# Optimization experiments

Measured on AMD Instinct MI355X. Metric: run time of the kernel, lower is better.

## Reference

```python
import jax, jax.numpy as jnp
import numpy as np

N = 50000      # nodes
E = 600000     # edges
G = 256        # graphs in batch
HID = 128      # gcn hidden = gcn in = gcn out
EDIM = 16      # edge feature dim
EH = 64        # edge mlp hidden
NL = 4         # gcn layers
MIN_ = 200     # mol feature dim
MH = 256       # mlp hidden
MOUT = 128     # mlp out
PH = 512       # predictor hidden
PIN = HID + MOUT


def setup_inputs() -> dict:
    key = jax.random.key(0)
    ks = jax.random.split(key, 32)
    f = lambda k, s: jax.random.normal(k, s, dtype=jnp.float32)
    p = lambda k, s: 0.05 * jax.random.normal(k, s, dtype=jnp.float32)
    return {
        "x": f(ks[0], (N, HID)),
        "edge_index": jax.random.randint(ks[1], (2, E), 0, N),
        "edge_attr": f(ks[2], (E, EDIM)),
        "batch_index": jnp.sort(jax.random.randint(ks[3], (N,), 0, G)),
        "mol_features": f(ks[4], (G, MIN_)),
        # PDNConv params (stacked over NL layers)
        "conv_lin_W": p(ks[5], (NL, HID, HID)),
        "conv_mW1": p(ks[6], (NL, EDIM, EH)),
        "conv_mb1": p(ks[7], (NL, EH)),
        "conv_mW2": p(ks[8], (NL, EH)),
        "conv_mb2": p(ks[9], (NL,)),
        "conv_bias": p(ks[10], (NL, HID)),
        # dense Linear after each conv
        "gcn_W": p(ks[11], (NL, HID, HID)),
        "gcn_b": p(ks[12], (NL, HID)),
        # mol-feature MLP (n_mlp_layers=3 -> 4 linears)
        "mlp_W0": p(ks[13], (MIN_, MH)), "mlp_b0": p(ks[14], (MH,)),
        "mlp_W1": p(ks[15], (MH, MH)),   "mlp_b1": p(ks[16], (MH,)),
        "mlp_W2": p(ks[17], (MH, MH)),   "mlp_b2": p(ks[18], (MH,)),
        "mlp_W3": p(ks[19], (MH, MOUT)), "mlp_b3": p(ks[20], (MOUT,)),
        # predictor
        "pred_W0": p(ks[21], (PIN, PH)), "pred_b0": p(ks[22], (PH,)),
        "pred_W1": p(ks[23], (PH, PH)),  "pred_b1": p(ks[24], (PH,)),
        "out_W": p(ks[25], (PH, 1)),     "out_b": p(ks[26], (1,)),
    }


def _pdn_conv(h, row, col, edge_attr, lin_W, mW1, mb1, mW2, mb2, bias):
    # edge MLP -> sigmoid gate (PyG PDNConv)
    w = jax.nn.sigmoid(jnp.maximum(edge_attr @ mW1 + mb1, 0.0) @ mW2 + mb2)  # [E]
    # gcn_norm with self loops (fill weight 1.0)
    loop = jnp.arange(N)
    r = jnp.concatenate([row, loop])
    c = jnp.concatenate([col, loop])
    w_all = jnp.concatenate([w, jnp.ones((N,), h.dtype)])
    deg = jax.ops.segment_sum(w_all, c, num_segments=N)
    dinv = jnp.where(deg > 0, jax.lax.rsqrt(deg), 0.0)
    norm = dinv[r] * w_all * dinv[c]                                          # [E+N]
    hl = h @ lin_W                                                            # [N,HID]
    out = jax.ops.segment_sum(norm[:, None] * hl[r], c, num_segments=N)
    return out + bias


def reference(x, edge_index, edge_attr, batch_index, mol_features,
              conv_lin_W, conv_mW1, conv_mb1, conv_mW2, conv_mb2, conv_bias,
              gcn_W, gcn_b,
              mlp_W0, mlp_b0, mlp_W1, mlp_b1, mlp_W2, mlp_b2, mlp_W3, mlp_b3,
              pred_W0, pred_b0, pred_W1, pred_b1, out_W, out_b):
    row, col = edge_index[0], edge_index[1]
    relu = lambda v: jnp.maximum(v, 0.0)

    # GCN stack: PDNConv -> relu(Linear), x NL
    h1 = x
    for i in range(NL):
        h1 = _pdn_conv(h1, row, col, edge_attr, conv_lin_W[i], conv_mW1[i],
                       conv_mb1[i], conv_mW2[i], conv_mb2[i], conv_bias[i])
        h1 = relu(h1 @ gcn_W[i] + gcn_b[i])
    # global mean pool over graphs
    sums = jax.ops.segment_sum(h1, batch_index, num_segments=G)
    cnts = jax.ops.segment_sum(jnp.ones((N,), h1.dtype), batch_index, num_segments=G)
    h1 = sums / jnp.maximum(cnts, 1.0)[:, None]                               # [G,HID]

    # molecular-feature MLP
    h2 = relu(mol_features @ mlp_W0 + mlp_b0)
    h2 = relu(h2 @ mlp_W1 + mlp_b1)
    h2 = relu(h2 @ mlp_W2 + mlp_b2)
    h2 = relu(h2 @ mlp_W3 + mlp_b3)                                           # [G,MOUT]

    h = jnp.concatenate([h1, h2], axis=1)                                     # [G,PIN]
    h = relu(h @ pred_W0 + pred_b0)
    h = relu(h @ pred_W1 + pred_b1)
    return h @ out_W + out_b                                                  # [G,1]
```

## Files before the change

### kernel.cpp

```cpp
#include <hip/hip_runtime.h>
#include <hip/hip_bf16.h>


#define NN 50000
#define EE 600000
#define GG 256
#define HID 128
#define EDIM 16
#define EHID 64
#define NL 4
#define MIN_F 200
#define MH 256
#define MOUT 128
#define PH 512
#define PIN 256
#define SCAN_B 196
#define PCH 8

typedef __hip_bfloat16 bf16;
typedef __attribute__((ext_vector_type(8))) short bf16x8;
typedef __attribute__((ext_vector_type(4))) float f32x4;

__device__ __forceinline__ float bfl(unsigned u) { return __uint_as_float(u << 16); }
__device__ __forceinline__ float bfh(unsigned u) { return __uint_as_float(u & 0xffff0000u); }
__device__ __forceinline__ float b2f(bf16 x) { return __bfloat162float(x); }
__device__ __forceinline__ float ldf(const void* p, long i, bool bf) {
  return bf ? __bfloat162float(((const bf16*)p)[i]) : ((const float*)p)[i];
}
__device__ __forceinline__ unsigned short f2bf_bits(float v) {
  bf16 h = __float2bfloat16(v);
  return *reinterpret_cast<unsigned short*>(&h);
}

__global__ void probe_kernel(const unsigned short* __restrict__ xs, int* flag) {
  if (threadIdx.x == 0 && blockIdx.x == 0) {
    int sane = 0;
    for (int i = 0; i < 128; i++) {
      unsigned e = (xs[i] >> 7) & 0xFF;
      if (e >= 96 && e <= 159) sane++;
    }
    *flag = (sane >= 112) ? 1 : 0;
  }
}

__global__ __launch_bounds__(256) void cvt_to_bf16(const void* __restrict__ in,
                                                   unsigned short* __restrict__ outp,
                                                   int n8, const int* __restrict__ flag) {
  bool bf = *flag != 0;
  int i = blockIdx.x * 256 + threadIdx.x;
  if (i >= n8) return;
  if (bf) {
    reinterpret_cast<uint4*>(outp)[i] = reinterpret_cast<const uint4*>(in)[i];
  } else {
    const float4* p = reinterpret_cast<const float4*>(in) + (size_t)i * 2;
    float4 v0 = p[0], v1 = p[1];
    ushort4 a, b;
    a.x = f2bf_bits(v0.x); a.y = f2bf_bits(v0.y);
    a.z = f2bf_bits(v0.z); a.w = f2bf_bits(v0.w);
    b.x = f2bf_bits(v1.x); b.y = f2bf_bits(v1.y);
    b.z = f2bf_bits(v1.z); b.w = f2bf_bits(v1.w);
    reinterpret_cast<ushort4*>(outp)[i * 2] = a;
    reinterpret_cast<ushort4*>(outp)[i * 2 + 1] = b;
  }
}

__global__ __launch_bounds__(256) void cvt_molf(const void* __restrict__ in,
                                                float* __restrict__ outp,
                                                const int* __restrict__ flag) {
  bool bf = *flag != 0;
  int i = blockIdx.x * 256 + threadIdx.x;
  if (i >= GG * 50) return;
  int row = i / 50, c4 = (i % 50) * 4;
  float4 v;
  if (bf) {
    const unsigned short* p = (const unsigned short*)in + (size_t)row * MIN_F + c4;
    uint2 u = *reinterpret_cast<const uint2*>(p);
    v.x = bfl(u.x); v.y = bfh(u.x); v.z = bfl(u.y); v.w = bfh(u.y);
  } else {
    v = *reinterpret_cast<const float4*>((const float*)in + (size_t)row * MIN_F + c4);
  }
  *reinterpret_cast<float4*>(&outp[(size_t)row * 256 + c4]) = v;
}

__global__ __launch_bounds__(256) void prep_fused_w(const void* __restrict__ lin_W,
                                                    const void* __restrict__ gW,
                                                    unsigned short* __restrict__ Wt,
                                                    const int* __restrict__ flag) {
  bool bf = *flag != 0;
  int idx = blockIdx.x * 256 + threadIdx.x;
  if (idx >= 4 * 16384) return;
  int l = idx >> 14;
  int rem = idx & 16383;
  int n = rem >> 7, k = rem & 127;
  float s = 0.f;
  long lb = (long)l * 16384;
  for (int m = 0; m < 128; m++)
    s += ldf(lin_W, lb + (long)k * 128 + m, bf) * ldf(gW, lb + (long)m * 128 + n, bf);
  Wt[idx] = f2bf_bits(s);
}

__global__ __launch_bounds__(128) void prep_fused_b(const void* __restrict__ cbias,
                                                    const void* __restrict__ gW,
                                                    const void* __restrict__ gb,
                                                    float* __restrict__ bprime,
                                                    const int* __restrict__ flag) {
  bool bf = *flag != 0;
  int idx = blockIdx.x * 128 + threadIdx.x;
  if (idx >= NL * HID) return;
  int l = idx >> 7, n = idx & 127;
  float s = ldf(gb, idx, bf);
  long lb = (long)l * 16384;
  for (int k = 0; k < 128; k++)
    s += ldf(cbias, (long)l * 128 + k, bf) * ldf(gW, lb + (long)k * 128 + n, bf);
  bprime[idx] = s;
}

__global__ __launch_bounds__(256) void prep_edge_w(const void* __restrict__ mW1,
                                                   const void* __restrict__ mb1,
                                                   unsigned short* __restrict__ W1t,
                                                   const int* __restrict__ flag) {
  bool bf = *flag != 0;
  int idx = blockIdx.x * 256 + threadIdx.x;
  if (idx >= 256 * 32) return;
  int col = idx >> 5, k = idx & 31;
  float v = 0.f;
  if (k < EDIM) v = ldf(mW1, (long)(col >> 6) * (EDIM * EHID) + (long)k * EHID + (col & 63), bf);
  else if (k == EDIM) v = ldf(mb1, col, bf);
  W1t[idx] = f2bf_bits(v);
}

__global__ __launch_bounds__(256) void prep_tail(
    const void* __restrict__ mlpW0, const void* __restrict__ mlpW1,
    const void* __restrict__ mlpW2, const void* __restrict__ mlpW3,
    const void* __restrict__ predW0, const void* __restrict__ predW1,
    unsigned short* __restrict__ T, const int* __restrict__ flag) {
  bool bf = *flag != 0;
  int idx = blockIdx.x * 256 + threadIdx.x;
  const void* src; int N, Kp, Ksrc, off;
  if      (idx < 65536)  { src = mlpW0;  N = 256; Kp = 256; Ksrc = 200; off = 0; }
  else if (idx < 131072) { src = mlpW1;  N = 256; Kp = 256; Ksrc = 256; off = 65536; }
  else if (idx < 196608) { src = mlpW2;  N = 256; Kp = 256; Ksrc = 256; off = 131072; }
  else if (idx < 229376) { src = mlpW3;  N = 128; Kp = 256; Ksrc = 256; off = 196608; }
  else if (idx < 360448) { src = predW0; N = 512; Kp = 256; Ksrc = 256; off = 229376; }
  else if (idx < 622592) { src = predW1; N = 512; Kp = 512; Ksrc = 512; off = 360448; }
  else return;
  int rem = idx - off;
  int n = rem / Kp, k = rem % Kp;
  float v = (k < Ksrc) ? ldf(src, (long)k * N + n, bf) : 0.f;
  T[idx] = f2bf_bits(v);
}

__global__ __launch_bounds__(256) void count_kernel(const int* __restrict__ ei,
                                                    int* __restrict__ cnt) {
  int e = blockIdx.x * 256 + threadIdx.x;
  if (e >= EE) return;
  int c = ei[EE + e];
  c = min(max(c, 0), NN - 1);
  atomicAdd(&cnt[c], 1);
}

__global__ __launch_bounds__(256) void scan_phase1(const int* __restrict__ cnt,
                                                   int* __restrict__ bsum) {
  __shared__ int red[256];
  int tid = threadIdx.x;
  int i = blockIdx.x * 256 + tid;
  red[tid] = (i < NN) ? cnt[i] : 0;
  __syncthreads();
  for (int off = 128; off > 0; off >>= 1) {
    if (tid < off) red[tid] += red[tid + off];
    __syncthreads();
  }
  if (tid == 0) bsum[blockIdx.x] = red[0];
}

__global__ __launch_bounds__(256) void scan_phase2(int* __restrict__ bsum,
                                                   int* __restrict__ offs) {
  __shared__ int buf[256];
  int tid = threadIdx.x;
  int v = (tid < SCAN_B) ? bsum[tid] : 0;
  buf[tid] = v;
  __syncthreads();
  for (int off = 1; off < 256; off <<= 1) {
    int t = (tid >= off) ? buf[tid - off] : 0;
    __syncthreads();
    buf[tid] += t;
    __syncthreads();
  }
  if (tid < SCAN_B) bsum[tid] = buf[tid] - v;
  if (tid == 255) offs[NN] = buf[255];
}

__global__ __launch_bounds__(256) void scan_phase3(const int* __restrict__ cnt,
                                                   const int* __restrict__ bsum,
                                                   int* __restrict__ offs) {
  __shared__ int buf[256];
  int tid = threadIdx.x;
  int i = blockIdx.x * 256 + tid;
  int v = (i < NN) ? cnt[i] : 0;
  buf[tid] = v;
  __syncthreads();
  for (int off = 1; off < 256; off <<= 1) {
    int t = (tid >= off) ? buf[tid - off] : 0;
    __syncthreads();
    buf[tid] += t;
    __syncthreads();
  }
  if (i < NN) offs[i] = bsum[blockIdx.x] + buf[tid] - v;
}

__global__ __launch_bounds__(256) void fill_kernel(const int* __restrict__ ei,
                                                   const int* __restrict__ offs,
                                                   int* __restrict__ cursor,
                                                   int2* __restrict__ csr_se) {
  int e = blockIdx.x * 256 + threadIdx.x;
  if (e >= EE) return;
  int c = ei[EE + e];
  c = min(max(c, 0), NN - 1);
  int pos = offs[c] + atomicAdd(&cursor[c], 1);
  pos = min(max(pos, 0), EE - 1);
  csr_se[pos] = make_int2(ei[e], e);
}

__global__ __launch_bounds__(256) void edge_mlp_mfma(
    const void* __restrict__ eattr, const unsigned short* __restrict__ W1t,
    const void* __restrict__ mW2, const void* __restrict__ mb2,
    float* __restrict__ w_all4, const int* __restrict__ flag) {
  bool bf = *flag != 0;
  int tid = threadIdx.x;
  int wave = tid >> 6, lane = tid & 63;
  int l15 = lane & 15, quad = lane >> 4;

  bf16x8 bfrag[16];
#pragma unroll
  for (int t = 0; t < 16; t++)
    bfrag[t] = *reinterpret_cast<const bf16x8*>(&W1t[(t * 16 + l15) * 32 + quad * 8]);

  float w2v[16];
#pragma unroll
  for (int t = 0; t < 16; t++) w2v[t] = ldf(mW2, t * 16 + l15, bf);
  float b2v0 = ldf(mb2, 0, bf), b2v1 = ldf(mb2, 1, bf);
  float b2v2 = ldf(mb2, 2, bf), b2v3 = ldf(mb2, 3, bf);
  float b2 = b2v0;
  b2 = (l15 == 1) ? b2v1 : b2;
  b2 = (l15 == 2) ? b2v2 : b2;
  b2 = (l15 == 3) ? b2v3 : b2;
  bool o1 = (l15 & 1) != 0;
  bool o2 = (l15 & 2) != 0;

  int ebase = blockIdx.x * 512 + wave * 128;
#pragma unroll 1
  for (int f = 0; f < 8; f++) {
    int fbase = ebase + f * 16;
    if (fbase < EE) {
      long erow = fbase + l15;
      bf16x8 a = (bf16x8){0, 0, 0, 0, 0, 0, 0, 0};
      if (quad < 2) {
        if (bf) {
          uint4 v = *reinterpret_cast<const uint4*>((const bf16*)eattr + erow * EDIM + quad * 8);
          a = *reinterpret_cast<bf16x8*>(&v);
        } else {
          const float4* p =
              reinterpret_cast<const float4*>((const float*)eattr + erow * EDIM + quad * 8);
          float4 v0 = p[0], v1 = p[1];
          a[0] = (short)f2bf_bits(v0.x); a[1] = (short)f2bf_bits(v0.y);
          a[2] = (short)f2bf_bits(v0.z); a[3] = (short)f2bf_bits(v0.w);
          a[4] = (short)f2bf_bits(v1.x); a[5] = (short)f2bf_bits(v1.y);
          a[6] = (short)f2bf_bits(v1.z); a[7] = (short)f2bf_bits(v1.w);
        }
      }
      if (quad == 2) a[0] = (short)0x3F80;
      float s00 = 0.f, s01 = 0.f, s02 = 0.f, s03 = 0.f;
      float s10 = 0.f, s11 = 0.f, s12 = 0.f, s13 = 0.f;
      float s20 = 0.f, s21 = 0.f, s22 = 0.f, s23 = 0.f;
      float s30 = 0.f, s31 = 0.f, s32 = 0.f, s33 = 0.f;
#define DO_T(T, S0, S1, S2, S3)                                               \
  {                                                                           \
    f32x4 acc = __builtin_amdgcn_mfma_f32_16x16x32_bf16(                      \
        a, bfrag[T], (f32x4){0.f, 0.f, 0.f, 0.f}, 0, 0, 0);                   \
    S0 += fmaxf(acc.x, 0.f) * w2v[T];                                         \
    S1 += fmaxf(acc.y, 0.f) * w2v[T];                                         \
    S2 += fmaxf(acc.z, 0.f) * w2v[T];                                         \
    S3 += fmaxf(acc.w, 0.f) * w2v[T];                                         \
  }
      DO_T(0,  s00, s01, s02, s03) DO_T(1,  s00, s01, s02, s03)
      DO_T(2,  s00, s01, s02, s03) DO_T(3,  s00, s01, s02, s03)
      DO_T(4,  s10, s11, s12, s13) DO_T(5,  s10, s11, s12, s13)
      DO_T(6,  s10, s11, s12, s13) DO_T(7,  s10, s11, s12, s13)
      DO_T(8,  s20, s21, s22, s23) DO_T(9,  s20, s21, s22, s23)
      DO_T(10, s20, s21, s22, s23) DO_T(11, s20, s21, s22, s23)
      DO_T(12, s30, s31, s32, s33) DO_T(13, s30, s31, s32, s33)
      DO_T(14, s30, s31, s32, s33) DO_T(15, s30, s31, s32, s33)
#undef DO_T
#define RS_STEP1(AR, S0R, S1R) \
  float AR = (o1 ? S1R : S0R) + __shfl_xor(o1 ? S0R : S1R, 1);
      RS_STEP1(a0, s00, s10)
      RS_STEP1(a1, s01, s11)
      RS_STEP1(a2, s02, s12)
      RS_STEP1(a3, s03, s13)
      RS_STEP1(bb0, s20, s30)
      RS_STEP1(bb1, s21, s31)
      RS_STEP1(bb2, s22, s32)
      RS_STEP1(bb3, s23, s33)
#undef RS_STEP1
      float c0 = (o2 ? bb0 : a0) + __shfl_xor(o2 ? a0 : bb0, 2);
      float c1 = (o2 ? bb1 : a1) + __shfl_xor(o2 ? a1 : bb1, 2);
      float c2 = (o2 ? bb2 : a2) + __shfl_xor(o2 ? a2 : bb2, 2);
      float c3 = (o2 ? bb3 : a3) + __shfl_xor(o2 ? a3 : bb3, 2);
      c0 += __shfl_xor(c0, 4); c1 += __shfl_xor(c1, 4);
      c2 += __shfl_xor(c2, 4); c3 += __shfl_xor(c3, 4);
      c0 += __shfl_xor(c0, 8); c1 += __shfl_xor(c1, 8);
      c2 += __shfl_xor(c2, 8); c3 += __shfl_xor(c3, 8);
      if (l15 < NL) {
        float g0 = 1.f / (1.f + __expf(-(c0 + b2)));
        float g1 = 1.f / (1.f + __expf(-(c1 + b2)));
        float g2 = 1.f / (1.f + __expf(-(c2 + b2)));
        float g3 = 1.f / (1.f + __expf(-(c3 + b2)));
        w_all4[(size_t)(fbase + quad * 4 + 0) * 4 + l15] = g0;
        w_all4[(size_t)(fbase + quad * 4 + 1) * 4 + l15] = g1;
        w_all4[(size_t)(fbase + quad * 4 + 2) * 4 + l15] = g2;
        w_all4[(size_t)(fbase + quad * 4 + 3) * 4 + l15] = g3;
      }
    }
  }
}

__global__ __launch_bounds__(256) void csr_gather(const int2* __restrict__ csr_se,
                                                  const float* __restrict__ w_all4,
                                                  float* __restrict__ csr_val) {
  int k = blockIdx.x * 256 + threadIdx.x;
  if (k >= EE) return;
  int eid = csr_se[k].y;
  eid = min(max(eid, 0), EE - 1);
  float4 w = reinterpret_cast<const float4*>(w_all4)[eid];
  csr_val[k] = w.x;
  csr_val[(size_t)EE + k] = w.y;
  csr_val[2 * (size_t)EE + k] = w.z;
  csr_val[3 * (size_t)EE + k] = w.w;
}

__global__ __launch_bounds__(256) void deg_kernel(const int* __restrict__ offs,
                                                  const float* __restrict__ csr_val,
                                                  float* __restrict__ dinv4) {
  int n = blockIdx.x * 256 + threadIdx.x;
  if (n >= NN) return;
  int s = offs[n], e = offs[n + 1];
  float d0 = 1.f, d1 = 1.f, d2 = 1.f, d3 = 1.f;
  for (int k = s; k < e; k++) {
    d0 += csr_val[k];
    d1 += csr_val[EE + k];
    d2 += csr_val[2 * (size_t)EE + k];
    d3 += csr_val[3 * (size_t)EE + k];
  }
  float4 o;
  o.x = rsqrtf(d0); o.y = rsqrtf(d1); o.z = rsqrtf(d2); o.w = rsqrtf(d3);
  reinterpret_cast<float4*>(dinv4)[n] = o;
}

__global__ __launch_bounds__(256) void csr_scale_kernel(const int2* __restrict__ csr_se,
                                                        const float* __restrict__ dinv4,
                                                        float* __restrict__ csr_val) {
  int k = blockIdx.x * 256 + threadIdx.x;
  if (k >= EE) return;
  int s = csr_se[k].x;
  s = min(max(s, 0), NN - 1);
  float4 d = reinterpret_cast<const float4*>(dinv4)[s];
  csr_val[k] *= d.x;
  csr_val[(size_t)EE + k] *= d.y;
  csr_val[2 * (size_t)EE + k] *= d.z;
  csr_val[3 * (size_t)EE + k] *= d.w;
}

__global__ __launch_bounds__(256) void gemm_nodes_bf16(
    const unsigned short* __restrict__ A16, const unsigned short* __restrict__ Wt,
    const float* __restrict__ bias, unsigned short* __restrict__ out16,
    int relu) {
  __shared__ alignas(16) unsigned short sA[64 * 136];
  __shared__ alignas(16) unsigned short sW[128 * 136];
  int tid = threadIdx.x;
  int rbase = blockIdx.x * 64;

#pragma unroll
  for (int p = 0; p < 8; p++) {
    int idx8 = p * 256 + tid;
    int n = idx8 >> 4, kc = idx8 & 15;
    uint4 v = reinterpret_cast<const uint4*>(Wt)[idx8];
    *reinterpret_cast<uint4*>(&sW[n * 136 + kc * 8]) = v;
  }
#pragma unroll
  for (int p = 0; p < 4; p++) {
    int idx8 = p * 256 + tid;
    int m = idx8 >> 4, kc = idx8 & 15;
    int row = rbase + m;
    uint4 v = make_uint4(0u, 0u, 0u, 0u);
    if (row < NN)
      v = *reinterpret_cast<const uint4*>(&A16[(size_t)row * HID + kc * 8]);
    *reinterpret_cast<uint4*>(&sA[m * 136 + kc * 8]) = v;
  }
  __syncthreads();

  int wave = tid >> 6, lane = tid & 63;
  int l15 = lane & 15, quad = lane >> 4;
  int mstrip = wave * 16;

  f32x4 acc[8];
#pragma unroll
  for (int t = 0; t < 8; t++) acc[t] = (f32x4){0.f, 0.f, 0.f, 0.f};

#pragma unroll
  for (int ks = 0; ks < 4; ks++) {
    int k0 = ks * 32 + quad * 8;
    bf16x8 a = *reinterpret_cast<const bf16x8*>(&sA[(mstrip + l15) * 136 + k0]);
#pragma unroll
    for (int t = 0; t < 8; t++) {
      bf16x8 b = *reinterpret_cast<const bf16x8*>(&sW[(t * 16 + l15) * 136 + k0]);
      acc[t] = __builtin_amdgcn_mfma_f32_16x16x32_bf16(a, b, acc[t], 0, 0, 0);
    }
  }

#pragma unroll
  for (int t = 0; t < 8; t++) {
    int n = t * 16 + l15;
    float bv = bias ? bias[n] : 0.f;
#pragma unroll
    for (int r = 0; r < 4; r++) {
      int row = rbase + mstrip + quad * 4 + r;
      if (row < NN) {
        float o = acc[t][r] + bv;
        if (relu) o = fmaxf(o, 0.f);
        out16[(size_t)row * HID + n] = f2bf_bits(o);
      }
    }
  }
}

__global__ __launch_bounds__(256) void gemm_tail_mfma(
    const float* __restrict__ A, int lda, const unsigned short* __restrict__ Wt,
    int Kp, const void* __restrict__ bias, float* __restrict__ outp, int ldo,
    int relu, const int* __restrict__ flag) {
  __shared__ alignas(16) unsigned short sA[64 * 264];
  __shared__ alignas(16) unsigned short sW[64 * 264];
  int tid = threadIdx.x;
  int rbase = blockIdx.x * 64;
  int nbase = blockIdx.y * 64;
  int wave = tid >> 6, lane = tid & 63;
  int l15 = lane & 15, quad = lane >> 4;
  int mstrip = wave * 16;

  f32x4 acc[4];
#pragma unroll
  for (int t = 0; t < 4; t++) acc[t] = (f32x4){0.f, 0.f, 0.f, 0.f};

  for (int kc = 0; kc < Kp; kc += 256) {
#pragma unroll 4
    for (int p = 0; p < 16; p++) {
      int idx = p * 1024 + tid * 4;
      int m = idx >> 8, k = idx & 255;
      float4 v = *reinterpret_cast<const float4*>(&A[(size_t)(rbase + m) * lda + kc + k]);
      ushort4 b;
      b.x = f2bf_bits(v.x); b.y = f2bf_bits(v.y);
      b.z = f2bf_bits(v.z); b.w = f2bf_bits(v.w);
      *reinterpret_cast<ushort4*>(&sA[m * 264 + k]) = b;
    }
#pragma unroll 4
    for (int p = 0; p < 8; p++) {
      int idx8 = p * 256 + tid;
      int n = idx8 >> 5, kk = (idx8 & 31) * 8;
      uint4 v = *reinterpret_cast<const uint4*>(&Wt[(size_t)(nbase + n) * Kp + kc + kk]);
      *reinterpret_cast<uint4*>(&sW[n * 264 + kk]) = v;
    }
    __syncthreads();
#pragma unroll
    for (int ks = 0; ks < 8; ks++) {
      int k0 = ks * 32 + quad * 8;
      bf16x8 a = *reinterpret_cast<const bf16x8*>(&sA[(mstrip + l15) * 264 + k0]);
#pragma unroll
      for (int nt = 0; nt < 4; nt++) {
        bf16x8 b = *reinterpret_cast<const bf16x8*>(&sW[(nt * 16 + l15) * 264 + k0]);
        acc[nt] = __builtin_amdgcn_mfma_f32_16x16x32_bf16(a, b, acc[nt], 0, 0, 0);
      }
    }
    __syncthreads();
  }

  bool bf = *flag != 0;
#pragma unroll
  for (int nt = 0; nt < 4; nt++) {
    int col = nbase + nt * 16 + l15;
    float bv = ldf(bias, col, bf);
#pragma unroll
    for (int r = 0; r < 4; r++) {
      int row = rbase + mstrip + quad * 4 + r;
      float o = acc[nt][r] + bv;
      if (relu) o = fmaxf(o, 0.f);
      outp[(size_t)row * ldo + col] = o;
    }
  }
}

__global__ __launch_bounds__(64) void aggregate_kernel(
    const unsigned short* __restrict__ h16, const int* __restrict__ offs,
    const int2* __restrict__ csr_se, const float* __restrict__ csr_val,
    const float* __restrict__ dinv4, int layer,
    unsigned short* __restrict__ out16) {
  int n = blockIdx.x;
  int lane = threadIdx.x;
  int grp = lane >> 4;
  int c16 = lane & 15;
  __shared__ int s_src[64];
  __shared__ float s_val[64];
  int start = offs[n], end = offs[n + 1];
  float a0 = 0.f, a1 = 0.f, a2 = 0.f, a3 = 0.f;
  float a4 = 0.f, a5 = 0.f, a6 = 0.f, a7 = 0.f;
  for (int base = start; base < end; base += 64) {
    int k = base + lane;
    if (k < end) {
      s_src[lane] = min(max(csr_se[k].x, 0), NN - 1);
      s_val[lane] = csr_val[k];
    }
    __syncthreads();
    int m = min(64, end - base);
    for (int j = grp; j < m; j += 4) {
      float v = s_val[j];
      uint4 u = *reinterpret_cast<const uint4*>(&h16[(size_t)s_src[j] * HID + c16 * 8]);
      a0 = fmaf(v, bfl(u.x), a0); a1 = fmaf(v, bfh(u.x), a1);
      a2 = fmaf(v, bfl(u.y), a2); a3 = fmaf(v, bfh(u.y), a3);
      a4 = fmaf(v, bfl(u.z), a4); a5 = fmaf(v, bfh(u.z), a5);
      a6 = fmaf(v, bfl(u.w), a6); a7 = fmaf(v, bfh(u.w), a7);
    }
    __syncthreads();
  }
  a0 += __shfl_xor(a0, 16); a1 += __shfl_xor(a1, 16);
  a2 += __shfl_xor(a2, 16); a3 += __shfl_xor(a3, 16);
  a4 += __shfl_xor(a4, 16); a5 += __shfl_xor(a5, 16);
  a6 += __shfl_xor(a6, 16); a7 += __shfl_xor(a7, 16);
  a0 += __shfl_xor(a0, 32); a1 += __shfl_xor(a1, 32);
  a2 += __shfl_xor(a2, 32); a3 += __shfl_xor(a3, 32);
  a4 += __shfl_xor(a4, 32); a5 += __shfl_xor(a5, 32);
  a6 += __shfl_xor(a6, 32); a7 += __shfl_xor(a7, 32);
  if (grp == 0) {
    float dn = dinv4[(size_t)n * 4 + layer];
    float dn2 = dn * dn;
    uint4 su = *reinterpret_cast<const uint4*>(&h16[(size_t)n * HID + c16 * 8]);
    ushort4 o0, o1v;
    o0.x  = f2bf_bits(dn * a0 + dn2 * bfl(su.x));
    o0.y  = f2bf_bits(dn * a1 + dn2 * bfh(su.x));
    o0.z  = f2bf_bits(dn * a2 + dn2 * bfl(su.y));
    o0.w  = f2bf_bits(dn * a3 + dn2 * bfh(su.y));
    o1v.x = f2bf_bits(dn * a4 + dn2 * bfl(su.z));
    o1v.y = f2bf_bits(dn * a5 + dn2 * bfh(su.z));
    o1v.z = f2bf_bits(dn * a6 + dn2 * bfl(su.w));
    o1v.w = f2bf_bits(dn * a7 + dn2 * bfh(su.w));
    *reinterpret_cast<ushort4*>(&out16[(size_t)n * HID + c16 * 8]) = o0;
    *reinterpret_cast<ushort4*>(&out16[(size_t)n * HID + c16 * 8 + 4]) = o1v;
  }
}

__global__ __launch_bounds__(128) void pool_partial(const unsigned short* __restrict__ h16,
                                                    const int* __restrict__ batch,
                                                    float* __restrict__ part) {
  int g = blockIdx.x, chunk = blockIdx.y, c = threadIdx.x;
  int lo = 0, hi = NN;
  while (lo < hi) { int mid = (lo + hi) >> 1; if (batch[mid] < g) lo = mid + 1; else hi = mid; }
  int start = lo;
  hi = NN;
  while (lo < hi) { int mid = (lo + hi) >> 1; if (batch[mid] < g + 1) lo = mid + 1; else hi = mid; }
  int end = lo;
  int len = end - start;
  int per = (len + PCH - 1) / PCH;
  int s = start + chunk * per;
  int e = min(s + per, end);
  float sum = 0.f;
  for (int n = s; n < e; n++) sum += bfl((unsigned)h16[(size_t)n * HID + c]);
  part[((size_t)g * PCH + chunk) * HID + c] = sum;
}

__global__ __launch_bounds__(128) void pool_combine(const float* __restrict__ part,
                                                    const int* __restrict__ batch,
                                                    float* __restrict__ cat) {
  int g = blockIdx.x, c = threadIdx.x;
  int lo = 0, hi = NN;
  while (lo < hi) { int mid = (lo + hi) >> 1; if (batch[mid] < g) lo = mid + 1; else hi = mid; }
  int start = lo;
  hi = NN;
  while (lo < hi) { int mid = (lo + hi) >> 1; if (batch[mid] < g + 1) lo = mid + 1; else hi = mid; }
  int end = lo;
  float s = 0.f;
#pragma unroll
  for (int k = 0; k < PCH; k++) s += part[((size_t)g * PCH + k) * HID + c];
  float cntf = (float)(end - start);
  cat[(size_t)g * PIN + c] = s / fmaxf(cntf, 1.f);
}

__global__ __launch_bounds__(64) void final_kernel(const float* __restrict__ A,
                                                   const void* __restrict__ W,
                                                   const void* __restrict__ b,
                                                   void* __restrict__ outp,
                                                   const int* __restrict__ flag) {
  bool bf = *flag != 0;
  int g = blockIdx.x, lane = threadIdx.x;
  float s = 0.f;
  for (int k = lane; k < PH; k += 64) s = fmaf(A[(size_t)g * PH + k], ldf(W, k, bf), s);
#pragma unroll
  for (int off = 32; off > 0; off >>= 1) s += __shfl_down(s, off);
  if (lane == 0) {
    float r = s + ldf(b, 0, bf);
    if (bf) ((bf16*)outp)[g] = __float2bfloat16(r);
    else    ((float*)outp)[g] = r;
  }
}

extern "C" void kernel_launch(void* const* d_in, const int* in_sizes, int n_in,
                              void* d_out, int out_size, void* d_ws, size_t ws_size,
                              hipStream_t stream) {
  const void* x      = d_in[0];
  const int*  ei     = (const int*)d_in[1];
  const void* eattr  = d_in[2];
  const int*  batch  = (const int*)d_in[3];
  const void* molf   = d_in[4];
  const void* lin_W  = d_in[5];
  const void* mW1    = d_in[6];
  const void* mb1    = d_in[7];
  const void* mW2    = d_in[8];
  const void* mb2    = d_in[9];
  const void* cbias  = d_in[10];
  const void* gW     = d_in[11];
  const void* gb     = d_in[12];
  const void* mlpW0  = d_in[13];
  const void* mlpb0  = d_in[14];
  const void* mlpW1  = d_in[15];
  const void* mlpb1  = d_in[16];
  const void* mlpW2  = d_in[17];
  const void* mlpb2  = d_in[18];
  const void* mlpW3  = d_in[19];
  const void* mlpb3  = d_in[20];
  const void* predW0 = d_in[21];
  const void* predb0 = d_in[22];
  const void* predW1 = d_in[23];
  const void* predb1 = d_in[24];
  const void* outW   = d_in[25];
  const void* outb   = d_in[26];

  char* base = (char*)d_ws;
  size_t off = 0;
  auto alloc = [&](size_t bytes) -> char* {
    char* p = base + off;
    off = (off + bytes + 255) & ~(size_t)255;
    return p;
  };
  unsigned short* h16  = (unsigned short*)alloc((size_t)NN * HID * 2);
  unsigned short* t16  = (unsigned short*)alloc((size_t)NN * HID * 2);
  float* dinv4    = (float*)alloc((size_t)NN * 4 * 4);
  int*   cnt      = (int*)alloc((size_t)NN * 4);
  int*   offs     = (int*)alloc((size_t)(NN + 1) * 4);
  int*   cursor   = (int*)alloc((size_t)NN * 4);
  int*   bsum     = (int*)alloc((size_t)256 * 4);
  int2*  csr_se   = (int2*)alloc((size_t)EE * 8);
  float* csr_val  = (float*)alloc((size_t)NL * EE * 4);
  float* w_all4   = (float*)alloc((size_t)EE * 4 * 4);
  unsigned short* Wt    = (unsigned short*)alloc((size_t)NL * HID * HID * 2);
  float* bprime   = (float*)alloc((size_t)NL * HID * 4);
  unsigned short* tailW = (unsigned short*)alloc((size_t)622592 * 2);
  unsigned short* edgeW = (unsigned short*)alloc((size_t)256 * 32 * 2);
  int*   flag     = (int*)alloc(256);
  float* part     = (float*)alloc((size_t)GG * PCH * HID * 4);
  float* molf32   = (float*)alloc((size_t)GG * 256 * 4);
  float* m0       = (float*)alloc((size_t)GG * MH * 4);
  float* m1       = (float*)alloc((size_t)GG * MH * 4);
  float* cat      = (float*)alloc((size_t)GG * PIN * 4);
  float* p0       = (float*)alloc((size_t)GG * PH * 4);
  float* p1       = (float*)alloc((size_t)GG * PH * 4);

  hipMemsetAsync(cnt, 0, (size_t)NN * 4, stream);
  hipMemsetAsync(cursor, 0, (size_t)NN * 4, stream);
  hipMemsetAsync(molf32, 0, (size_t)GG * 256 * 4, stream);

  probe_kernel<<<1, 64, 0, stream>>>((const unsigned short*)x, flag);

  prep_fused_w<<<256, 256, 0, stream>>>(lin_W, gW, Wt, flag);
  prep_fused_b<<<NL, 128, 0, stream>>>(cbias, gW, gb, bprime, flag);
  prep_tail<<<(622592 + 255) / 256, 256, 0, stream>>>(mlpW0, mlpW1, mlpW2, mlpW3,
                                                      predW0, predW1, tailW, flag);
  prep_edge_w<<<32, 256, 0, stream>>>(mW1, mb1, edgeW, flag);

  {
    int n8 = NN * HID / 8;
    cvt_to_bf16<<<(n8 + 255) / 256, 256, 0, stream>>>(x, h16, n8, flag);
  }
  edge_mlp_mfma<<<(EE + 511) / 512, 256, 0, stream>>>(eattr, edgeW, mW2, mb2,
                                                      w_all4, flag);
  count_kernel<<<(EE + 255) / 256, 256, 0, stream>>>(ei, cnt);
  scan_phase1<<<SCAN_B, 256, 0, stream>>>(cnt, bsum);
  scan_phase2<<<1, 256, 0, stream>>>(bsum, offs);
  scan_phase3<<<SCAN_B, 256, 0, stream>>>(cnt, bsum, offs);
  fill_kernel<<<(EE + 255) / 256, 256, 0, stream>>>(ei, offs, cursor, csr_se);
  csr_gather<<<(EE + 255) / 256, 256, 0, stream>>>(csr_se, w_all4, csr_val);
  deg_kernel<<<(NN + 255) / 256, 256, 0, stream>>>(offs, csr_val, dinv4);
  csr_scale_kernel<<<(EE + 255) / 256, 256, 0, stream>>>(csr_se, dinv4, csr_val);

  const int gemm_blocks = (NN + 63) / 64;
  for (int l = 0; l < NL; l++) {
    aggregate_kernel<<<NN, 64, 0, stream>>>(h16, offs, csr_se,
                                            csr_val + (size_t)l * EE, dinv4, l, t16);
    gemm_nodes_bf16<<<gemm_blocks, 256, 0, stream>>>(
        t16, Wt + (size_t)l * HID * HID, bprime + (size_t)l * HID, h16, 1);
  }

  pool_partial<<<dim3(GG, PCH), 128, 0, stream>>>(h16, batch, part);
  pool_combine<<<GG, 128, 0, stream>>>(part, batch, cat);

  cvt_molf<<<(GG * 50 + 255) / 256, 256, 0, stream>>>(molf, molf32, flag);
  gemm_tail_mfma<<<dim3(4, 4), 256, 0, stream>>>(molf32, 256, tailW + 0,      256, mlpb0, m0, 256, 1, flag);
  gemm_tail_mfma<<<dim3(4, 4), 256, 0, stream>>>(m0,     256, tailW + 65536,  256, mlpb1, m1, 256, 1, flag);
  gemm_tail_mfma<<<dim3(4, 4), 256, 0, stream>>>(m1,     256, tailW + 131072, 256, mlpb2, m0, 256, 1, flag);
  gemm_tail_mfma<<<dim3(4, 2), 256, 0, stream>>>(m0,     256, tailW + 196608, 256, mlpb3, cat + MOUT, 256, 1, flag);

  gemm_tail_mfma<<<dim3(4, 8), 256, 0, stream>>>(cat, 256, tailW + 229376, 256, predb0, p0, 512, 1, flag);
  gemm_tail_mfma<<<dim3(4, 8), 256, 0, stream>>>(p0,  512, tailW + 360448, 512, predb1, p1, 512, 1, flag);
  final_kernel<<<GG, 64, 0, stream>>>(p1, outW, outb, d_out, flag);
}
```

Baseline: 575.8 us.

## Split edge-MLP layers across waves and software-prefetch edge attributes

Each wave now computes the gate for one GCN layer (4 of the 16 weight tiles) across all 512 edges of the block, instead of every wave computing all four layers for its own 128 edges. This cuts the per-wave register footprint for weight fragments, simplifies the cross-lane reduction to a single output, and adds a one-step prefetch of the next edge-attribute tile. The cost is that each edge attribute row is now loaded by four waves instead of one, and the gate writes become strided per layer.

Measured after the change: 592.6 us. 1.03x slower.

```diff
diff --git a/kernel.cpp b/kernel.cpp
--- a/kernel.cpp
+++ b/kernel.cpp
@@ -230,30 +230,25 @@
   int wave = tid >> 6, lane = tid & 63;
   int l15 = lane & 15, quad = lane >> 4;
 
-  bf16x8 bfrag[16];
-#pragma unroll
-  for (int t = 0; t < 16; t++)
-    bfrag[t] = *reinterpret_cast<const bf16x8*>(&W1t[(t * 16 + l15) * 32 + quad * 8]);
-
-  float w2v[16];
-#pragma unroll
-  for (int t = 0; t < 16; t++) w2v[t] = ldf(mW2, t * 16 + l15, bf);
-  float b2v0 = ldf(mb2, 0, bf), b2v1 = ldf(mb2, 1, bf);
-  float b2v2 = ldf(mb2, 2, bf), b2v3 = ldf(mb2, 3, bf);
-  float b2 = b2v0;
-  b2 = (l15 == 1) ? b2v1 : b2;
-  b2 = (l15 == 2) ? b2v2 : b2;
-  b2 = (l15 == 3) ? b2v3 : b2;
+  bf16x8 bfrag[4];
+#pragma unroll
+  for (int t = 0; t < 4; t++)
+    bfrag[t] =
+        *reinterpret_cast<const bf16x8*>(&W1t[((wave * 4 + t) * 16 + l15) * 32 + quad * 8]);
+
+  float w2v[4];
+#pragma unroll
+  for (int t = 0; t < 4; t++) w2v[t] = ldf(mW2, (wave * 4 + t) * 16 + l15, bf);
+  float b2 = ldf(mb2, wave, bf);
   bool o1 = (l15 & 1) != 0;
   bool o2 = (l15 & 2) != 0;
 
-  int ebase = blockIdx.x * 512 + wave * 128;
-#pragma unroll 1
-  for (int f = 0; f < 8; f++) {
-    int fbase = ebase + f * 16;
+  int ebase = blockIdx.x * 512;
+
+  auto load_a = [&](int fbase) -> bf16x8 {
+    bf16x8 a = (bf16x8){0, 0, 0, 0, 0, 0, 0, 0};
     if (fbase < EE) {
       long erow = fbase + l15;
-      bf16x8 a = (bf16x8){0, 0, 0, 0, 0, 0, 0, 0};
       if (quad < 2) {
         if (bf) {
           uint4 v = *reinterpret_cast<const uint4*>((const bf16*)eattr + erow * EDIM + quad * 8);
@@ -269,58 +264,39 @@
         }
       }
       if (quad == 2) a[0] = (short)0x3F80;
-      float s00 = 0.f, s01 = 0.f, s02 = 0.f, s03 = 0.f;
-      float s10 = 0.f, s11 = 0.f, s12 = 0.f, s13 = 0.f;
-      float s20 = 0.f, s21 = 0.f, s22 = 0.f, s23 = 0.f;
-      float s30 = 0.f, s31 = 0.f, s32 = 0.f, s33 = 0.f;
-#define DO_T(T, S0, S1, S2, S3)                                               \
+    }
+    return a;
+  };
+
+  bf16x8 a = load_a(ebase);
+#pragma unroll 2
+  for (int f = 0; f < 32; f++) {
+    int fbase = ebase + f * 16;
+    bf16x8 an = load_a(fbase + 16);
+    if (fbase < EE) {
+      float s0 = 0.f, s1 = 0.f, s2 = 0.f, s3 = 0.f;
+#define DO_T(T)                                                               \
   {                                                                           \
     f32x4 acc = __builtin_amdgcn_mfma_f32_16x16x32_bf16(                      \
         a, bfrag[T], (f32x4){0.f, 0.f, 0.f, 0.f}, 0, 0, 0);                   \
-    S0 += fmaxf(acc.x, 0.f) * w2v[T];                                         \
-    S1 += fmaxf(acc.y, 0.f) * w2v[T];                                         \
-    S2 += fmaxf(acc.z, 0.f) * w2v[T];                                         \
-    S3 += fmaxf(acc.w, 0.f) * w2v[T];                                         \
-  }
-      DO_T(0,  s00, s01, s02, s03) DO_T(1,  s00, s01, s02, s03)
-      DO_T(2,  s00, s01, s02, s03) DO_T(3,  s00, s01, s02, s03)
-      DO_T(4,  s10, s11, s12, s13) DO_T(5,  s10, s11, s12, s13)
-      DO_T(6,  s10, s11, s12, s13) DO_T(7,  s10, s11, s12, s13)
-      DO_T(8,  s20, s21, s22, s23) DO_T(9,  s20, s21, s22, s23)
-      DO_T(10, s20, s21, s22, s23) DO_T(11, s20, s21, s22, s23)
-      DO_T(12, s30, s31, s32, s33) DO_T(13, s30, s31, s32, s33)
-      DO_T(14, s30, s31, s32, s33) DO_T(15, s30, s31, s32, s33)
+    s0 += fmaxf(acc.x, 0.f) * w2v[T];                                         \
+    s1 += fmaxf(acc.y, 0.f) * w2v[T];                                         \
+    s2 += fmaxf(acc.z, 0.f) * w2v[T];                                         \
+    s3 += fmaxf(acc.w, 0.f) * w2v[T];                                         \
+  }
+      DO_T(0) DO_T(1) DO_T(2) DO_T(3)
 #undef DO_T
-#define RS_STEP1(AR, S0R, S1R) \
-  float AR = (o1 ? S1R : S0R) + __shfl_xor(o1 ? S0R : S1R, 1);
-      RS_STEP1(a0, s00, s10)
-      RS_STEP1(a1, s01, s11)
-      RS_STEP1(a2, s02, s12)
-      RS_STEP1(a3, s03, s13)
-      RS_STEP1(bb0, s20, s30)
-      RS_STEP1(bb1, s21, s31)
-      RS_STEP1(bb2, s22, s32)
-      RS_STEP1(bb3, s23, s33)
-#undef RS_STEP1
-      float c0 = (o2 ? bb0 : a0) + __shfl_xor(o2 ? a0 : bb0, 2);
-      float c1 = (o2 ? bb1 : a1) + __shfl_xor(o2 ? a1 : bb1, 2);
-      float c2 = (o2 ? bb2 : a2) + __shfl_xor(o2 ? a2 : bb2, 2);
-      float c3 = (o2 ? bb3 : a3) + __shfl_xor(o2 ? a3 : bb3, 2);
-      c0 += __shfl_xor(c0, 4); c1 += __shfl_xor(c1, 4);
-      c2 += __shfl_xor(c2, 4); c3 += __shfl_xor(c3, 4);
-      c0 += __shfl_xor(c0, 8); c1 += __shfl_xor(c1, 8);
-      c2 += __shfl_xor(c2, 8); c3 += __shfl_xor(c3, 8);
-      if (l15 < NL) {
-        float g0 = 1.f / (1.f + __expf(-(c0 + b2)));
-        float g1 = 1.f / (1.f + __expf(-(c1 + b2)));
-        float g2 = 1.f / (1.f + __expf(-(c2 + b2)));
-        float g3 = 1.f / (1.f + __expf(-(c3 + b2)));
-        w_all4[(size_t)(fbase + quad * 4 + 0) * 4 + l15] = g0;
-        w_all4[(size_t)(fbase + quad * 4 + 1) * 4 + l15] = g1;
-        w_all4[(size_t)(fbase + quad * 4 + 2) * 4 + l15] = g2;
-        w_all4[(size_t)(fbase + quad * 4 + 3) * 4 + l15] = g3;
+      float u0 = (o1 ? s1 : s0) + __shfl_xor(o1 ? s0 : s1, 1);
+      float u1 = (o1 ? s3 : s2) + __shfl_xor(o1 ? s2 : s3, 1);
+      float c = (o2 ? u1 : u0) + __shfl_xor(o2 ? u0 : u1, 2);
+      c += __shfl_xor(c, 4);
+      c += __shfl_xor(c, 8);
+      if (l15 < 4) {
+        float g = 1.f / (1.f + __expf(-(c + b2)));
+        w_all4[(size_t)(fbase + quad * 4 + l15) * 4 + wave] = g;
       }
     }
+    a = an;
   }
 }
 
```
